# Kernel optimization log

Hardware: AMD Instinct MI355X
Metric: run time of the kernel (lower is better)

Reference implementation:

```python
import jax, jax.numpy as jnp
import numpy as np

M = 262144          # rows of A == prod(out_shape) == 512*512
N = 262144          # cols of A == prod(x.shape)
NNZ = 8388608       # 32 nonzeros per row on average
OUT_SHAPE = (512, 512)


def setup_inputs() -> dict:
    key = jax.random.key(0)
    k1, k2, k3, k4 = jax.random.split(key, 4)
    A_rows = jax.random.randint(k1, (NNZ,), 0, M, dtype=jnp.int32)
    A_cols = jax.random.randint(k2, (NNZ,), 0, N, dtype=jnp.int32)
    A_vals = jax.random.normal(k3, (NNZ,), dtype=jnp.float32)
    x = jax.random.normal(k4, OUT_SHAPE, dtype=jnp.float32)
    return {"x": x, "A_vals": A_vals, "A_rows": A_rows, "A_cols": A_cols}


def reference(x, A_vals, A_rows, A_cols):
    # x.reshape(A.shape[1], 1); torch.sparse.mm(A, x); reshape(out_shape)
    xf = x.reshape(-1)                                   # [N]
    contrib = A_vals * jnp.take(xf, A_cols)              # [NNZ] gather + multiply
    y = jax.ops.segment_sum(contrib, A_rows, num_segments=M)  # scatter-add over rows
    return y.reshape(OUT_SHAPE).astype(jnp.float32)
```

## Files before the change

### kernel.cpp

```cpp
#include <hip/hip_runtime.h>


#define BINS_MAXB   64
#define ROW_SHIFT   13
#define ROWS_PER_BIN 8192
#define ENT         4096
#define SLICES      16


__global__ __launch_bounds__(256) void zero_out_kernel(float* __restrict__ y, int n) {
    int i = blockIdx.x * blockDim.x + threadIdx.x;
    if (i < n) y[i] = 0.0f;
}

__global__ __launch_bounds__(256) void spmv_coo_scatter(
    const float* __restrict__ vals, const int* __restrict__ rows,
    const int* __restrict__ cols, const float* __restrict__ x,
    float* __restrict__ y, int nnz)
{
    int i = (blockIdx.x * blockDim.x + threadIdx.x) * 4;
    if (i + 3 < nnz) {
        float4 v = *reinterpret_cast<const float4*>(vals + i);
        int4   r = *reinterpret_cast<const int4*>(rows + i);
        int4   c = *reinterpret_cast<const int4*>(cols + i);
        atomicAdd(&y[r.x], v.x * x[c.x]);
        atomicAdd(&y[r.y], v.y * x[c.y]);
        atomicAdd(&y[r.z], v.z * x[c.z]);
        atomicAdd(&y[r.w], v.w * x[c.w]);
    } else {
        for (; i < nnz; ++i) atomicAdd(&y[rows[i]], vals[i] * x[cols[i]]);
    }
}


__global__ __launch_bounds__(64) void init_cursors(unsigned* __restrict__ gcur, int bins) {
    int t = threadIdx.x;
    if (t < bins) gcur[t] = 0u;
}

__global__ __launch_bounds__(256) void scatter2_kernel(
    const int*   __restrict__ rows, const int* __restrict__ cols,
    const float* __restrict__ vals, const float* __restrict__ x, int nnz,
    unsigned* __restrict__ gcur, unsigned cap,
    unsigned short* __restrict__ okeys, float* __restrict__ ocontrib, int bins)
{
    __shared__ unsigned cnt[BINS_MAXB], lstart[BINS_MAXB], sresv[BINS_MAXB];
    __shared__ int dstb[BINS_MAXB];
    __shared__ unsigned cur2[BINS_MAXB];
    __shared__ unsigned total_s;
    __shared__ unsigned short skey[ENT];
    __shared__ float          sval[ENT];
    __shared__ unsigned char  sbin[ENT];

    const int t = threadIdx.x;
    for (int i = t; i < bins; i += 256) cnt[i] = 0u;
    __syncthreads();

    const int seg = blockIdx.x * ENT;

    int   rr[16];
    float ff[16];

    #pragma unroll
    for (int ch = 0; ch < 4; ++ch) {
        int base = seg + ch * 1024 + t * 4;
        if (base + 3 < nnz) {
            int4   r4 = *reinterpret_cast<const int4*>(rows + base);
            int4   c4 = *reinterpret_cast<const int4*>(cols + base);
            float4 v4 = *reinterpret_cast<const float4*>(vals + base);
            rr[ch*4+0] = r4.x; ff[ch*4+0] = v4.x * x[c4.x];
            rr[ch*4+1] = r4.y; ff[ch*4+1] = v4.y * x[c4.y];
            rr[ch*4+2] = r4.z; ff[ch*4+2] = v4.z * x[c4.z];
            rr[ch*4+3] = r4.w; ff[ch*4+3] = v4.w * x[c4.w];
        } else {
            #pragma unroll
            for (int j = 0; j < 4; ++j) {
                int idx = base + j;
                if (idx < nnz) { rr[ch*4+j] = rows[idx]; ff[ch*4+j] = vals[idx] * x[cols[idx]]; }
                else           { rr[ch*4+j] = -1; ff[ch*4+j] = 0.0f; }
            }
        }
    }
    #pragma unroll
    for (int j = 0; j < 16; ++j)
        if (rr[j] >= 0) atomicAdd(&cnt[rr[j] >> ROW_SHIFT], 1u);
    __syncthreads();

    if (t < bins) sresv[t] = atomicAdd(&gcur[t], cnt[t]);
    if (t == 0) {
        unsigned run = 0;
        for (int b = 0; b < bins; ++b) { lstart[b] = run; run += cnt[b]; }
        total_s = run;
    }
    __syncthreads();
    if (t < bins) {
        dstb[t] = (int)sresv[t] - (int)lstart[t];
        cur2[t] = lstart[t];
    }
    __syncthreads();

    #pragma unroll
    for (int j = 0; j < 16; ++j) {
        if (rr[j] >= 0) {
            int b = rr[j] >> ROW_SHIFT;
            unsigned p = atomicAdd(&cur2[b], 1u);
            skey[p] = (unsigned short)(rr[j] & (ROWS_PER_BIN - 1));
            sval[p] = ff[j];
            sbin[p] = (unsigned char)b;
        }
    }
    __syncthreads();

    const unsigned total = total_s;
    for (unsigned i = t; i < total; i += 256) {
        int b = sbin[i];
        unsigned off = (unsigned)(dstb[b] + (int)i);
        if (off < cap) {
            size_t dst = (size_t)b * cap + off;
            okeys[dst]    = skey[i];
            ocontrib[dst] = sval[i];
        }
    }
}

__global__ __launch_bounds__(256) void accum2_kernel(
    const unsigned short* __restrict__ okeys, const float* __restrict__ ocontrib,
    const unsigned* __restrict__ gcur, unsigned cap,
    float* __restrict__ partials)
{
    __shared__ float acc[ROWS_PER_BIN];
    const int t = threadIdx.x;
    const int bin = blockIdx.x / SLICES;
    const int sl  = blockIdx.x % SLICES;

    #pragma unroll
    for (int i = 0; i < ROWS_PER_BIN / 256; ++i) acc[t + i * 256] = 0.0f;
    __syncthreads();

    unsigned count = gcur[bin];
    if (count > cap) count = cap;
    unsigned chunk = (count + SLICES - 1) / SLICES;
    chunk = (chunk + 3u) & ~3u;
    unsigned lo = (unsigned)sl * chunk;
    unsigned hi = lo + chunk; if (hi > count) hi = count;

    const unsigned short* k = okeys    + (size_t)bin * cap;
    const float*          c = ocontrib + (size_t)bin * cap;

    unsigned i = lo + (unsigned)t * 4u;
    for (; i + 3u < hi; i += 1024u) {
        ushort4 k4 = *reinterpret_cast<const ushort4*>(k + i);
        float4  c4 = *reinterpret_cast<const float4*>(c + i);
        atomicAdd(&acc[k4.x], c4.x);
        atomicAdd(&acc[k4.y], c4.y);
        atomicAdd(&acc[k4.z], c4.z);
        atomicAdd(&acc[k4.w], c4.w);
    }
    for (; i < hi; ++i) atomicAdd(&acc[k[i]], c[i]);
    __syncthreads();

    float* p = partials + (size_t)blockIdx.x * ROWS_PER_BIN;
    #pragma unroll
    for (int j = 0; j < ROWS_PER_BIN / 1024; ++j) {
        int l = j * 1024 + t * 4;
        *reinterpret_cast<float4*>(p + l) = *reinterpret_cast<const float4*>(&acc[l]);
    }
}

__global__ __launch_bounds__(256) void reduce2_kernel(
    const float* __restrict__ partials, float* __restrict__ y, int out_size)
{
    int r = blockIdx.x * 256 + threadIdx.x;
    if (r >= out_size) return;
    int bin = r >> ROW_SHIFT;
    int local = r & (ROWS_PER_BIN - 1);
    const float* p = partials + ((size_t)bin * SLICES) * ROWS_PER_BIN + local;
    float s = 0.0f;
    #pragma unroll
    for (int j = 0; j < SLICES; ++j) s += p[(size_t)j * ROWS_PER_BIN];
    y[r] = s;
}

extern "C" void kernel_launch(void* const* d_in, const int* in_sizes, int n_in,
                              void* d_out, int out_size, void* d_ws, size_t ws_size,
                              hipStream_t stream) {
    const float* x    = (const float*)d_in[0];
    const float* vals = (const float*)d_in[1];
    const int*   rows = (const int*)d_in[2];
    const int*   cols = (const int*)d_in[3];
    float* y = (float*)d_out;

    const int nnz  = in_sizes[1];
    const int bins = (out_size + ROWS_PER_BIN - 1) / ROWS_PER_BIN;
    const int nb   = (nnz + ENT - 1) / ENT;
    unsigned cap = (unsigned)(nnz / (bins > 0 ? bins : 1)) + 16384u;
    cap = (cap + 3u) & ~3u;

    auto align256 = [](size_t v) { return (v + 255) & ~(size_t)255; };
    size_t off_contrib  = 0;
    size_t off_keys     = align256(off_contrib + (size_t)bins * cap * 4);
    size_t off_partials = align256(off_keys + (size_t)bins * cap * 2);
    size_t off_gcur     = align256(off_partials + (size_t)bins * SLICES * ROWS_PER_BIN * 4);
    size_t need         = align256(off_gcur + (size_t)bins * 4);

    const bool ok = (bins >= 1) && (bins <= BINS_MAXB) && (need <= ws_size) && (nnz > 0);

    if (!ok) {
        zero_out_kernel<<<(out_size + 255) / 256, 256, 0, stream>>>(y, out_size);
        spmv_coo_scatter<<<(nnz + 1023) / 1024, 256, 0, stream>>>(vals, rows, cols, x, y, nnz);
        return;
    }

    char* w = (char*)d_ws;
    float*          ocontrib = (float*)(w + off_contrib);
    unsigned short* okeys    = (unsigned short*)(w + off_keys);
    float*          partials = (float*)(w + off_partials);
    unsigned*       gcur     = (unsigned*)(w + off_gcur);

    init_cursors<<<1, 64, 0, stream>>>(gcur, bins);
    scatter2_kernel<<<nb, 256, 0, stream>>>(rows, cols, vals, x, nnz, gcur, cap,
                                            okeys, ocontrib, bins);
    accum2_kernel<<<bins * SLICES, 256, 0, stream>>>(okeys, ocontrib, gcur, cap, partials);
    reduce2_kernel<<<(out_size + 255) / 256, 256, 0, stream>>>(partials, y, out_size);
}
```

Before: 230.9 us.

## Use 64 smaller row bins, per-wave LDS counters, smaller scatter tiles, vectorized reduce

Halves rows per bin to 4096, so 64 bins exist and the accumulation kernel launches 1024 blocks with a smaller LDS accumulator. The scatter kernel handles 2048 entries per block with 8 per thread and keeps per-wavefront bin counters and cursors to reduce LDS atomic contention, with launch bounds raised for occupancy. The reduce kernel reads and writes float4 vectors. Smaller scatter tiles mean more global cursor atomics and smaller contiguous write runs per bin.

```diff
diff --git a/kernel.cpp b/kernel.cpp
--- a/kernel.cpp
+++ b/kernel.cpp
@@ -1,11 +1,12 @@
 #include <hip/hip_runtime.h>
 
 
-#define BINS_MAXB   64
-#define ROW_SHIFT   13
-#define ROWS_PER_BIN 8192
-#define ENT         4096
-#define SLICES      16
+#define BINS         64
+#define ROW_SHIFT    12
+#define ROWS_PER_BIN 4096
+#define ENT          2048
+#define IPT          8
+#define SLICES       16
 
 
 __global__ __launch_bounds__(256) void zero_out_kernel(float* __restrict__ y, int n) {
@@ -33,36 +34,39 @@
 }
 
 
-__global__ __launch_bounds__(64) void init_cursors(unsigned* __restrict__ gcur, int bins) {
-    int t = threadIdx.x;
-    if (t < bins) gcur[t] = 0u;
-}
-
-__global__ __launch_bounds__(256) void scatter2_kernel(
+__global__ __launch_bounds__(64) void init_cursors(unsigned* __restrict__ gcur) {
+    gcur[threadIdx.x] = 0u;
+}
+
+__global__ __launch_bounds__(256, 8) void scatter3_kernel(
     const int*   __restrict__ rows, const int* __restrict__ cols,
     const float* __restrict__ vals, const float* __restrict__ x, int nnz,
     unsigned* __restrict__ gcur, unsigned cap,
-    unsigned short* __restrict__ okeys, float* __restrict__ ocontrib, int bins)
-{
-    __shared__ unsigned cnt[BINS_MAXB], lstart[BINS_MAXB], sresv[BINS_MAXB];
-    __shared__ int dstb[BINS_MAXB];
-    __shared__ unsigned cur2[BINS_MAXB];
+    unsigned short* __restrict__ okeys, float* __restrict__ ocontrib)
+{
+    __shared__ unsigned cnt[4 * BINS];
+    __shared__ unsigned cur2[4 * BINS];
+    __shared__ unsigned lstart[BINS];
+    __shared__ unsigned totbin[BINS];
+    __shared__ unsigned sresv[BINS];
+    __shared__ int      dstb[BINS];
     __shared__ unsigned total_s;
     __shared__ unsigned short skey[ENT];
     __shared__ float          sval[ENT];
     __shared__ unsigned char  sbin[ENT];
 
-    const int t = threadIdx.x;
-    for (int i = t; i < bins; i += 256) cnt[i] = 0u;
+    const int t   = threadIdx.x;
+    const int wid = t >> 6;
+    for (int i = t; i < 4 * BINS; i += 256) cnt[i] = 0u;
     __syncthreads();
 
     const int seg = blockIdx.x * ENT;
 
-    int   rr[16];
-    float ff[16];
-
-    #pragma unroll
-    for (int ch = 0; ch < 4; ++ch) {
+    int   rr[IPT];
+    float ff[IPT];
+
+    #pragma unroll
+    for (int ch = 0; ch < IPT / 4; ++ch) {
         int base = seg + ch * 1024 + t * 4;
         if (base + 3 < nnz) {
             int4   r4 = *reinterpret_cast<const int4*>(rows + base);
@@ -82,28 +86,37 @@
         }
     }
     #pragma unroll
-    for (int j = 0; j < 16; ++j)
-        if (rr[j] >= 0) atomicAdd(&cnt[rr[j] >> ROW_SHIFT], 1u);
-    __syncthreads();
-
-    if (t < bins) sresv[t] = atomicAdd(&gcur[t], cnt[t]);
+    for (int j = 0; j < IPT; ++j)
+        if (rr[j] >= 0) atomicAdd(&cnt[wid * BINS + (rr[j] >> ROW_SHIFT)], 1u);
+    __syncthreads();
+
+    if (t < BINS) {
+        unsigned tot = cnt[t] + cnt[BINS + t] + cnt[2 * BINS + t] + cnt[3 * BINS + t];
+        totbin[t] = tot;
+        sresv[t]  = atomicAdd(&gcur[t], tot);
+    }
+    __syncthreads();
     if (t == 0) {
         unsigned run = 0;
-        for (int b = 0; b < bins; ++b) { lstart[b] = run; run += cnt[b]; }
+        for (int b = 0; b < BINS; ++b) { lstart[b] = run; run += totbin[b]; }
         total_s = run;
     }
     __syncthreads();
-    if (t < bins) {
+    if (t < BINS) {
         dstb[t] = (int)sresv[t] - (int)lstart[t];
-        cur2[t] = lstart[t];
-    }
-    __syncthreads();
-
-    #pragma unroll
-    for (int j = 0; j < 16; ++j) {
+        unsigned o = lstart[t];
+        cur2[t] = o;            o += cnt[t];
+        cur2[BINS + t] = o;     o += cnt[BINS + t];
+        cur2[2 * BINS + t] = o; o += cnt[2 * BINS + t];
+        cur2[3 * BINS + t] = o;
+    }
+    __syncthreads();
+
+    #pragma unroll
+    for (int j = 0; j < IPT; ++j) {
         if (rr[j] >= 0) {
             int b = rr[j] >> ROW_SHIFT;
-            unsigned p = atomicAdd(&cur2[b], 1u);
+            unsigned p = atomicAdd(&cur2[wid * BINS + b], 1u);
             skey[p] = (unsigned short)(rr[j] & (ROWS_PER_BIN - 1));
             sval[p] = ff[j];
             sbin[p] = (unsigned char)b;
@@ -123,18 +136,21 @@
     }
 }
 
-__global__ __launch_bounds__(256) void accum2_kernel(
+__global__ __launch_bounds__(256) void accum3_kernel(
     const unsigned short* __restrict__ okeys, const float* __restrict__ ocontrib,
     const unsigned* __restrict__ gcur, unsigned cap,
     float* __restrict__ partials)
 {
     __shared__ float acc[ROWS_PER_BIN];
-    const int t = threadIdx.x;
+    const int t   = threadIdx.x;
     const int bin = blockIdx.x / SLICES;
     const int sl  = blockIdx.x % SLICES;
 
     #pragma unroll
-    for (int i = 0; i < ROWS_PER_BIN / 256; ++i) acc[t + i * 256] = 0.0f;
+    for (int i = 0; i < ROWS_PER_BIN / 1024; ++i) {
+        int l = i * 1024 + t * 4;
+        *reinterpret_cast<float4*>(&acc[l]) = make_float4(0.f, 0.f, 0.f, 0.f);
+    }
     __syncthreads();
 
     unsigned count = gcur[bin];
@@ -167,18 +183,29 @@
     }
 }
 
-__global__ __launch_bounds__(256) void reduce2_kernel(
+__global__ __launch_bounds__(256) void reduce3_kernel(
     const float* __restrict__ partials, float* __restrict__ y, int out_size)
 {
-    int r = blockIdx.x * 256 + threadIdx.x;
-    if (r >= out_size) return;
-    int bin = r >> ROW_SHIFT;
-    int local = r & (ROWS_PER_BIN - 1);
+    int r = (blockIdx.x * 256 + threadIdx.x) * 4;
+    if (r + 3 >= out_size) {
+        for (int q = r; q < out_size; ++q) {
+            int bin = q >> ROW_SHIFT, local = q & (ROWS_PER_BIN - 1);
+            const float* p = partials + ((size_t)bin * SLICES) * ROWS_PER_BIN + local;
+            float s = 0.f;
+            for (int j = 0; j < SLICES; ++j) s += p[(size_t)j * ROWS_PER_BIN];
+            y[q] = s;
+        }
+        return;
+    }
+    int bin = r >> ROW_SHIFT, local = r & (ROWS_PER_BIN - 1);
     const float* p = partials + ((size_t)bin * SLICES) * ROWS_PER_BIN + local;
-    float s = 0.0f;
-    #pragma unroll
-    for (int j = 0; j < SLICES; ++j) s += p[(size_t)j * ROWS_PER_BIN];
-    y[r] = s;
+    float4 s = make_float4(0.f, 0.f, 0.f, 0.f);
+    #pragma unroll
+    for (int j = 0; j < SLICES; ++j) {
+        float4 v = *reinterpret_cast<const float4*>(p + (size_t)j * ROWS_PER_BIN);
+        s.x += v.x; s.y += v.y; s.z += v.z; s.w += v.w;
+    }
+    *reinterpret_cast<float4*>(y + r) = s;
 }
 
 extern "C" void kernel_launch(void* const* d_in, const int* in_sizes, int n_in,
@@ -190,20 +217,20 @@
     const int*   cols = (const int*)d_in[3];
     float* y = (float*)d_out;
 
-    const int nnz  = in_sizes[1];
-    const int bins = (out_size + ROWS_PER_BIN - 1) / ROWS_PER_BIN;
-    const int nb   = (nnz + ENT - 1) / ENT;
-    unsigned cap = (unsigned)(nnz / (bins > 0 ? bins : 1)) + 16384u;
+    const int nnz = in_sizes[1];
+    const int nb  = (nnz + ENT - 1) / ENT;
+    unsigned cap = (unsigned)(nnz / BINS) + 8192u;
     cap = (cap + 3u) & ~3u;
 
     auto align256 = [](size_t v) { return (v + 255) & ~(size_t)255; };
     size_t off_contrib  = 0;
-    size_t off_keys     = align256(off_contrib + (size_t)bins * cap * 4);
-    size_t off_partials = align256(off_keys + (size_t)bins * cap * 2);
-    size_t off_gcur     = align256(off_partials + (size_t)bins * SLICES * ROWS_PER_BIN * 4);
-    size_t need         = align256(off_gcur + (size_t)bins * 4);
-
-    const bool ok = (bins >= 1) && (bins <= BINS_MAXB) && (need <= ws_size) && (nnz > 0);
+    size_t off_keys     = align256(off_contrib + (size_t)BINS * cap * 4);
+    size_t off_partials = align256(off_keys + (size_t)BINS * cap * 2);
+    size_t off_gcur     = align256(off_partials + (size_t)BINS * SLICES * ROWS_PER_BIN * 4);
+    size_t need         = align256(off_gcur + (size_t)BINS * 4);
+
+    const bool ok = (out_size <= BINS * ROWS_PER_BIN) && (out_size % 4 == 0) &&
+                    (need <= ws_size) && (nnz > 0);
 
     if (!ok) {
         zero_out_kernel<<<(out_size + 255) / 256, 256, 0, stream>>>(y, out_size);
@@ -217,9 +244,9 @@
     float*          partials = (float*)(w + off_partials);
     unsigned*       gcur     = (unsigned*)(w + off_gcur);
 
-    init_cursors<<<1, 64, 0, stream>>>(gcur, bins);
-    scatter2_kernel<<<nb, 256, 0, stream>>>(rows, cols, vals, x, nnz, gcur, cap,
-                                            okeys, ocontrib, bins);
-    accum2_kernel<<<bins * SLICES, 256, 0, stream>>>(okeys, ocontrib, gcur, cap, partials);
-    reduce2_kernel<<<(out_size + 255) / 256, 256, 0, stream>>>(partials, y, out_size);
-}
+    init_cursors<<<1, BINS, 0, stream>>>(gcur);
+    scatter3_kernel<<<nb, 256, 0, stream>>>(rows, cols, vals, x, nnz, gcur, cap,
+                                            okeys, ocontrib);
+    accum3_kernel<<<BINS * SLICES, 256, 0, stream>>>(okeys, ocontrib, gcur, cap, partials);
+    reduce3_kernel<<<(out_size / 4 + 255) / 256, 256, 0, stream>>>(partials, y, out_size);
+}
```

Result: slower. 253.8 us (+10.0%).
